# Kernel tuning notes

Measured on AMD Instinct MI355X. Metric: run time of the kernel, lower is better.

## Reference

```python
import jax, jax.numpy as jnp
import numpy as np

N_NODES = 50000
N_EDGES = 800000
D = 64
N_LAYERS = 3  # zip(convs(4), batchnorms(3)) truncates to 3 executed layers
N_GRAPHS = 32
EPS_BN = 1e-5
NEG_SLOPE = 0.2


def segment_softmax(logits, seg, n):
    m = jax.ops.segment_max(logits, seg, num_segments=n)
    m = jnp.where(jnp.isfinite(m), m, 0.0)
    z = jnp.exp(logits - m[seg])
    s = jax.ops.segment_sum(z, seg, num_segments=n)
    return z / (s[seg] + 1e-16)


def setup_inputs() -> dict:
    key = jax.random.key(0)
    ks = jax.random.split(key, 16)
    s = 0.1
    return {
        "x": jax.random.normal(ks[0], (N_NODES, D), jnp.float32),
        "edge_index": jax.random.randint(ks[1], (2, N_EDGES), 0, N_NODES),
        "edge_attr": jax.random.normal(ks[2], (N_EDGES, D), jnp.float32),
        "batch": jnp.sort(jax.random.randint(ks[3], (N_NODES,), 0, N_GRAPHS)),
        # EdgeConvLayer MLP params (stacked over layers)
        "em_w1": jax.random.normal(ks[4], (N_LAYERS, 3 * D, D)) * s,
        "em_b1": jnp.zeros((N_LAYERS, D)),
        "em_w2": jax.random.normal(ks[5], (N_LAYERS, D, D)) * s,
        "em_b2": jnp.zeros((N_LAYERS, D)),
        # GATConv params (heads=1, add_self_loops=False)
        "gat_w": jax.random.normal(ks[6], (N_LAYERS, D, D)) * s,
        "att_src": jax.random.normal(ks[7], (N_LAYERS, D)) * s,
        "att_dst": jax.random.normal(ks[8], (N_LAYERS, D)) * s,
        "edge_w": jax.random.normal(ks[9], (N_LAYERS, D, D)) * s,
        "att_edge": jax.random.normal(ks[10], (N_LAYERS, D)) * s,
        "gat_bias": jnp.zeros((N_LAYERS, D)),
        # BatchNorm params
        "bn_gamma": jnp.ones((N_LAYERS, D)),
        "bn_beta": jnp.zeros((N_LAYERS, D)),
        # readout MLP
        "mlp_w1": jax.random.normal(ks[11], (D, D)) * s,
        "mlp_b1": jnp.zeros((D,)),
        "mlp_w2": jax.random.normal(ks[12], (D, D // 2)) * s,
        "mlp_b2": jnp.zeros((D // 2,)),
        "mlp_w3": jax.random.normal(ks[13], (D // 2, 1)) * s,
        "mlp_b3": jnp.zeros((1,)),
    }


def reference(x, edge_index, edge_attr, batch, em_w1, em_b1, em_w2, em_b2,
              gat_w, att_src, att_dst, edge_w, att_edge, gat_bias,
              bn_gamma, bn_beta, mlp_w1, mlp_b1, mlp_w2, mlp_b2, mlp_w3, mlp_b3):
    row, col = edge_index[0], edge_index[1]
    n = x.shape[0]
    for l in range(N_LAYERS):
        # MetaLayer edge model: cat(src, dst, edge_attr) -> 2-layer MLP
        cat = jnp.concatenate([x[row], x[col], edge_attr], axis=1)  # (E, 3D)
        eh = jax.nn.relu(cat @ em_w1[l] + em_b1[l])
        edge_attr = eh @ em_w2[l] + em_b2[l]  # (E, D)
        # GATConv, heads=1: shared linear for src/dst
        xw = x @ gat_w[l]  # (N, D)
        a_edge = edge_attr @ (edge_w[l] @ att_edge[l])  # fused lin_edge + att_edge dot
        logits = (xw @ att_src[l])[row] + (xw @ att_dst[l])[col] + a_edge
        alpha = segment_softmax(jax.nn.leaky_relu(logits, NEG_SLOPE), col, n)
        h = jax.ops.segment_sum(alpha[:, None] * xw[row], col, num_segments=n) + gat_bias[l]
        # BatchNorm (training batch stats) + ReLU
        mu = h.mean(axis=0)
        var = h.var(axis=0)
        x = jax.nn.relu((h - mu) * jax.lax.rsqrt(var + EPS_BN) * bn_gamma[l] + bn_beta[l])
    # global mean pool over graphs
    sums = jax.ops.segment_sum(x, batch, num_segments=N_GRAPHS)
    cnt = jax.ops.segment_sum(jnp.ones((n,), x.dtype), batch, num_segments=N_GRAPHS)
    g = sums / jnp.maximum(cnt, 1.0)[:, None]
    h = jax.nn.relu(g @ mlp_w1 + mlp_b1)
    h = jax.nn.relu(h @ mlp_w2 + mlp_b2)
    return h @ mlp_w3 + mlp_b3  # (N_GRAPHS, 1)
```

## Files before the change

### kernel.cpp

```cpp
#include <hip/hip_runtime.h>


#define NN 50000
#define NE 800000
#define DP 68
#define NEG_SLOPE 0.2f

typedef __attribute__((ext_vector_type(8))) __bf16 bf16x8;
typedef __attribute__((ext_vector_type(4))) float f32x4;

__device__ __forceinline__ float4 ld4(const float* __restrict__ p){ return *(const float4* __restrict__)p; }
__device__ __forceinline__ void st4(float* __restrict__ p, float4 v){ *(float4* __restrict__)p = v; }
__device__ __forceinline__ float4 f4zero(){ return make_float4(0.f,0.f,0.f,0.f); }
__device__ __forceinline__ float4 f4add(float4 a, float4 b){
  return make_float4(a.x+b.x, a.y+b.y, a.z+b.z, a.w+b.w);
}
__device__ __forceinline__ float4 f4fma(float a, float4 b, float4 c){
  return make_float4(fmaf(a,b.x,c.x), fmaf(a,b.y,c.y), fmaf(a,b.z,c.z), fmaf(a,b.w,c.w));
}
__device__ __forceinline__ float f4dot(float4 a, float4 b){
  return fmaf(a.x,b.x, fmaf(a.y,b.y, fmaf(a.z,b.z, a.w*b.w)));
}
__device__ __forceinline__ bf16x8 cvt8(float4 a, float4 b){
  bf16x8 r;
  r[0]=(__bf16)a.x; r[1]=(__bf16)a.y; r[2]=(__bf16)a.z; r[3]=(__bf16)a.w;
  r[4]=(__bf16)b.x; r[5]=(__bf16)b.y; r[6]=(__bf16)b.z; r[7]=(__bf16)b.w;
  return r;
}
__device__ __forceinline__ bf16x8 addpack8(bf16x8 a, bf16x8 b){
  bf16x8 r;
#pragma unroll
  for (int e = 0; e < 8; ++e) r[e] = (__bf16)((float)a[e] + (float)b[e]);
  return r;
}
__device__ __forceinline__ ushort4 pack4(float4 v){
  ushort4 u;
  u.x = __builtin_bit_cast(unsigned short, (__bf16)v.x);
  u.y = __builtin_bit_cast(unsigned short, (__bf16)v.y);
  u.z = __builtin_bit_cast(unsigned short, (__bf16)v.z);
  u.w = __builtin_bit_cast(unsigned short, (__bf16)v.w);
  return u;
}
__device__ __forceinline__ float4 bnrelu4(float4 v, const float* sc, const float* sh, int d){
  return make_float4(
    fmaxf(fmaf(v.x, sc[d+0], sh[d+0]), 0.f),
    fmaxf(fmaf(v.y, sc[d+1], sh[d+1]), 0.f),
    fmaxf(fmaf(v.z, sc[d+2], sh[d+2]), 0.f),
    fmaxf(fmaf(v.w, sc[d+3], sh[d+3]), 0.f));
}

__device__ __forceinline__ void gemm_tile(const float* inT, const float* W,
                                          int el0, int d0, float4 acc[4]){
#pragma unroll 4
  for (int kc = 0; kc < 16; ++kc){
    float4 w0 = ld4(&W[(kc*4+0)*64 + d0]);
    float4 w1 = ld4(&W[(kc*4+1)*64 + d0]);
    float4 w2 = ld4(&W[(kc*4+2)*64 + d0]);
    float4 w3 = ld4(&W[(kc*4+3)*64 + d0]);
#pragma unroll
    for (int i = 0; i < 4; ++i){
      float4 iv = ld4(&inT[(el0+i)*DP + kc*4]);
      acc[i] = f4fma(iv.x, w0, acc[i]);
      acc[i] = f4fma(iv.y, w1, acc[i]);
      acc[i] = f4fma(iv.z, w2, acc[i]);
      acc[i] = f4fma(iv.w, w3, acc[i]);
    }
  }
}

__global__ __launch_bounds__(256) void hist_kernel(const int* __restrict__ ei_col,
                                                   int* __restrict__ cnt){
  int e = blockIdx.x * 256 + threadIdx.x;
  atomicAdd(&cnt[ei_col[e]], 1);
}

__global__ __launch_bounds__(256) void scan_kernel(const int* __restrict__ cnt,
                                                   int* __restrict__ off){
  __shared__ int wsum[4];
  __shared__ int carry_s;
  const int t = threadIdx.x;
  const int lane = t & 63, w = t >> 6;
  if (t == 0) carry_s = 0;
  __syncthreads();
  for (int base = 0; base < NN; base += 256){
    int idx = base + t;
    int v = (idx < NN) ? cnt[idx] : 0;
    int x = v;
#pragma unroll
    for (int o = 1; o < 64; o <<= 1){
      int u = __shfl_up(x, o);
      if (lane >= o) x += u;
    }
    if (lane == 63) wsum[w] = x;
    __syncthreads();
    int wo = carry_s;
#pragma unroll
    for (int k = 0; k < 4; ++k) if (k < w) wo += wsum[k];
    int incl = x + wo;
    if (idx < NN) off[idx] = incl - v;
    __syncthreads();
    if (t == 255) carry_s = incl;
    __syncthreads();
  }
  if (t == 0) off[NN] = carry_s;
}

__global__ __launch_bounds__(256) void scatter_kernel(
    const int* __restrict__ ei, const int* __restrict__ off, int* __restrict__ cur,
    int* __restrict__ srow, int* __restrict__ scol, int* __restrict__ perm){
  int e = blockIdx.x * 256 + threadIdx.x;
  int r = ei[e], c = ei[NE + e];
  int pos = off[c] + atomicAdd(&cur[c], 1);
  srow[pos] = r; scol[pos] = c; perm[pos] = e;
}

__global__ __launch_bounds__(256) void graph_bounds(const int* __restrict__ batch,
                                                    int* __restrict__ goff){
  int n = blockIdx.x * 256 + threadIdx.x;
  if (n >= NN) return;
  int bn = batch[n];
  int bp = (n == 0) ? -1 : batch[n-1];
  for (int g = bp + 1; g <= bn; ++g) goff[g] = n;
  if (n == NN - 1){ for (int g = bn + 1; g <= 32; ++g) goff[g] = NN; }
}

__global__ __launch_bounds__(256) void prep_weights(
    const float* __restrict__ em_w1, const float* __restrict__ em_w2,
    const float* __restrict__ edge_w, const float* __restrict__ att_edge,
    __bf16* __restrict__ w1f, __bf16* __restrict__ w2f, float* __restrict__ vbuf)
{
  const int l = blockIdx.x, t = threadIdx.x;
  const float* W1 = em_w1 + l*12288 + 8192;
  const float* W2 = em_w2 + l*4096;
  for (int p = t; p < 512; p += 256){
    int li = p & 63, ks = (p >> 6) & 1, nt = p >> 7;
    int kbase = ks*32 + (li >> 4)*8;
    int j = nt*16 + (li & 15);
    bf16x8 v1, v2;
#pragma unroll
    for (int e = 0; e < 8; ++e){
      v1[e] = (__bf16)W1[(size_t)(kbase+e)*64 + j];
      v2[e] = (__bf16)W2[(size_t)(kbase+e)*64 + j];
    }
    *(bf16x8*)(w1f + (size_t)l*4096 + p*8) = v1;
    *(bf16x8*)(w2f + (size_t)l*4096 + p*8) = v2;
  }
  if (t < 64){
    float a = 0.f;
    const float* ew = edge_w + l*4096 + t*64;
    const float* ae = att_edge + l*64;
#pragma unroll 8
    for (int j = 0; j < 64; ++j) a = fmaf(ew[j], ae[j], a);
    vbuf[l*64 + t] = a;
  }
}

__global__ __launch_bounds__(256) void node_prep(
    const float* __restrict__ x0_in, const float* __restrict__ h_in,
    const float* __restrict__ musum, const float* __restrict__ sqsum,
    const float* __restrict__ gamma, const float* __restrict__ beta,
    const float* __restrict__ em_w1, const float* __restrict__ em_b1,
    const float* __restrict__ gat_w,
    const float* __restrict__ att_src, const float* __restrict__ att_dst,
    __bf16* __restrict__ xaH, __bf16* __restrict__ xbH, __bf16* __restrict__ xwH,
    float* __restrict__ ssrc, float* __restrict__ sdst, int l)
{
  __shared__ float xt[64*DP];
  __shared__ float Ws[64*64];
  __shared__ float asrc[64], adst[64], b1s[64];
  __shared__ float sc[64], sh[64];
  const int t = threadIdx.x;
  const int n0 = blockIdx.x * 64;
  const int p = blockIdx.y;

  if (l > 0){
    if (t < 64){
      float mu  = musum[t] * (1.0f / NN);
      float var = sqsum[t] * (1.0f / NN) - mu * mu;
      float iv  = rsqrtf(var + 1e-5f) * gamma[(l-1)*64 + t];
      sc[t] = iv;
      sh[t] = beta[(l-1)*64 + t] - mu * iv;
    }
    __syncthreads();
  }

  { int nl = t >> 2, q = t & 3;
    int n = n0 + nl;
    float4 v0, v1, v2, v3;
    if (n < NN){
      const float* src = ((l == 0) ? x0_in : h_in) + (size_t)n*64 + q*16;
      v0 = ld4(src); v1 = ld4(src+4); v2 = ld4(src+8); v3 = ld4(src+12);
      if (l > 0){
        v0 = bnrelu4(v0, sc, sh, q*16);
        v1 = bnrelu4(v1, sc, sh, q*16+4);
        v2 = bnrelu4(v2, sc, sh, q*16+8);
        v3 = bnrelu4(v3, sc, sh, q*16+12);
      }
    } else { v0 = v1 = v2 = v3 = f4zero(); }
    float* dst = &xt[nl*DP + q*16];
    st4(dst, v0); st4(dst+4, v1); st4(dst+8, v2); st4(dst+12, v3);
  }
  if (p == 2){
    if (t < 64) asrc[t] = att_src[l*64 + t];
    else if (t < 128) adst[t-64] = att_dst[l*64 + (t-64)];
  } else if (p == 0 && t < 64){
    b1s[t] = em_b1[l*64 + t];
  }
  const float* wp = (p == 0) ? (em_w1 + l*12288)
                  : (p == 1) ? (em_w1 + l*12288 + 4096)
                             : (gat_w + l*4096);
  for (int i = t; i < 1024; i += 256) st4(&Ws[i*4], ld4(wp + i*4));
  __syncthreads();

  const int nl0 = (t >> 4) << 2;
  const int d0  = (t & 15) << 2;
  __bf16* op = (p == 0) ? xaH : (p == 1) ? xbH : xwH;

  float4 acc[4] = {f4zero(), f4zero(), f4zero(), f4zero()};
  gemm_tile(xt, Ws, nl0, d0, acc);
  if (p == 0){
    float4 bb = ld4(&b1s[d0]);
#pragma unroll
    for (int i = 0; i < 4; ++i) acc[i] = f4add(acc[i], bb);
  }
#pragma unroll
  for (int i = 0; i < 4; ++i){
    int n = n0 + nl0 + i;
    if (n < NN) *(ushort4*)(op + (size_t)n*64 + d0) = pack4(acc[i]);
  }
  if (p == 2){
    float4 a4 = ld4(&asrc[d0]);
    float4 b4 = ld4(&adst[d0]);
    float ps[4], pd[4];
#pragma unroll
    for (int i = 0; i < 4; ++i){ ps[i] = f4dot(acc[i], a4); pd[i] = f4dot(acc[i], b4); }
#pragma unroll
    for (int off = 8; off; off >>= 1){
#pragma unroll
      for (int i = 0; i < 4; ++i){ ps[i] += __shfl_xor(ps[i], off); pd[i] += __shfl_xor(pd[i], off); }
    }
    if ((t & 15) == 0){
#pragma unroll
      for (int i = 0; i < 4; ++i){
        int n = n0 + nl0 + i;
        if (n < NN){ ssrc[n] = ps[i]; sdst[n] = pd[i]; }
      }
    }
  }
}

__global__ __launch_bounds__(256) void edge_mlp(
    const float* __restrict__ ea0,
    const __bf16* ea_in,
    __bf16* ea_out,
    const __bf16* __restrict__ xaH, const __bf16* __restrict__ xbH,
    const float* __restrict__ ssrc, const float* __restrict__ sdst,
    const int* __restrict__ srow, const int* __restrict__ scol,
    const int* __restrict__ permp,
    const __bf16* __restrict__ w1f, const __bf16* __restrict__ w2f,
    const float* __restrict__ b2v, const float* __restrict__ vv,
    float* __restrict__ lrelu, int store_ea)
{
  __shared__ __align__(16) __bf16 uvh[64*72];
  __shared__ __align__(16) unsigned ehw[2048];
  __shared__ float b2s[64], vs[64], sb[128];
  __shared__ int rs[128], cs[128], ps[128];
  const int t = threadIdx.x;
  const int w = t >> 6, l = t & 63, m = l & 15, kg = l >> 4;
  const int eb = blockIdx.x * 128;

  if (t < 128){ rs[t] = srow[eb+t]; cs[t] = scol[eb+t]; }
  else if (t < 192){ b2s[t-128] = b2v[t-128]; vs[t-128] = vv[t-128]; }
  if (permp && t < 128) ps[t] = permp[eb+t];
  __syncthreads();

  const bf16x8* B1 = (const bf16x8*)w1f;
  const bf16x8* B2 = (const bf16x8*)w2f;
  const f32x4 z4 = {0.f, 0.f, 0.f, 0.f};
  const int e_loc = t >> 2, q = t & 3;

  const int r0 = rs[e_loc],      c0 = cs[e_loc];
  const int r1 = rs[64 + e_loc], c1 = cs[64 + e_loc];
  const bf16x8* pa0 = (const bf16x8*)(xaH + (size_t)r0*64 + q*16);
  const bf16x8* pb0 = (const bf16x8*)(xbH + (size_t)c0*64 + q*16);
  const bf16x8* pa1 = (const bf16x8*)(xaH + (size_t)r1*64 + q*16);
  const bf16x8* pb1 = (const bf16x8*)(xbH + (size_t)c1*64 + q*16);
  bf16x8 g_a0l = pa0[0], g_a0h = pa0[1], g_b0l = pb0[0], g_b0h = pb0[1];
  bf16x8 g_a1l = pa1[0], g_a1h = pa1[1], g_b1l = pb1[0], g_b1h = pb1[1];
  float sb0 = 0.f, sb1 = 0.f;
  if (q == 0){ sb0 = ssrc[r0] + sdst[c0]; sb1 = ssrc[r1] + sdst[c1]; }

  bf16x8 A00, A01, A10, A11;
  { const int elA = 16*w + m;
    if (ea0){
      const float* s0 = ea0 + (size_t)ps[elA]*64 + kg*8;
      const float* s1 = ea0 + (size_t)ps[64+elA]*64 + kg*8;
      A00 = cvt8(ld4(s0),    ld4(s0+4));  A01 = cvt8(ld4(s0+32), ld4(s0+36));
      A10 = cvt8(ld4(s1),    ld4(s1+4));  A11 = cvt8(ld4(s1+32), ld4(s1+36));
    } else {
      const __bf16* s0 = ea_in + (size_t)(eb+elA)*64 + kg*8;
      const __bf16* s1 = ea_in + (size_t)(eb+64+elA)*64 + kg*8;
      A00 = *(const bf16x8*)s0;  A01 = *(const bf16x8*)(s0+32);
      A10 = *(const bf16x8*)s1;  A11 = *(const bf16x8*)(s1+32);
    }
  }

  *(bf16x8*)&uvh[e_loc*72 + q*16]     = addpack8(g_a0l, g_b0l);
  *(bf16x8*)&uvh[e_loc*72 + q*16 + 8] = addpack8(g_a0h, g_b0h);
  if (q == 0){ sb[e_loc] = sb0; sb[64 + e_loc] = sb1; }
  asm volatile("" ::: "memory");

  __bf16* esc = (__bf16*)ehw;
  auto tile_compute = [&](bf16x8 a0, bf16x8 a1, int tb){
    f32x4 acc[4];
#pragma unroll
    for (int nt = 0; nt < 4; ++nt){
      acc[nt] = __builtin_amdgcn_mfma_f32_16x16x32_bf16(a0, B1[(nt*2+0)*64 + l], z4, 0, 0, 0);
      acc[nt] = __builtin_amdgcn_mfma_f32_16x16x32_bf16(a1, B1[(nt*2+1)*64 + l], acc[nt], 0, 0, 0);
    }
#pragma unroll
    for (int nt = 0; nt < 4; ++nt){
      const int j = nt*16 + m;
#pragma unroll
      for (int r = 0; r < 4; ++r){
        const int erow = 16*w + 4*kg + r;
        float v = acc[nt][r] + (float)uvh[erow*72 + j];
        v = fmaxf(v, 0.f);
        const int piece = (w*2 + (nt>>1))*64 + (((nt&1)<<1) | (m>>3))*16 + 4*kg + r;
        esc[piece*8 + (m&7)] = (__bf16)v;
      }
    }
    asm volatile("" ::: "memory");
    bf16x8 a20 = *(const bf16x8*)(esc + (size_t)((w*2+0)*64 + kg*16 + m)*8);
    bf16x8 a21 = *(const bf16x8*)(esc + (size_t)((w*2+1)*64 + kg*16 + m)*8);
    f32x4 acc2[4];
#pragma unroll
    for (int nt = 0; nt < 4; ++nt){
      acc2[nt] = __builtin_amdgcn_mfma_f32_16x16x32_bf16(a20, B2[(nt*2+0)*64 + l], z4, 0, 0, 0);
      acc2[nt] = __builtin_amdgcn_mfma_f32_16x16x32_bf16(a21, B2[(nt*2+1)*64 + l], acc2[nt], 0, 0, 0);
    }
    float p0 = 0.f, p1 = 0.f, p2 = 0.f, p3 = 0.f;
#pragma unroll
    for (int nt = 0; nt < 4; ++nt){
      const int j = nt*16 + m;
      const float bj = b2s[j], vj = vs[j];
      float vr[4];
      vr[0] = acc2[nt][0] + bj; vr[1] = acc2[nt][1] + bj;
      vr[2] = acc2[nt][2] + bj; vr[3] = acc2[nt][3] + bj;
      if (store_ea){
        const size_t rowb = (size_t)(eb + tb + 16*w + 4*kg)*64 + (j & ~1);
#pragma unroll
        for (int r = 0; r < 4; ++r){
          unsigned short hu = __builtin_bit_cast(unsigned short, (__bf16)vr[r]);
          int pu = __shfl_xor((int)hu, 1);
          if (!(m & 1)){
            unsigned word = (unsigned)hu | ((unsigned)(pu & 0xffff) << 16);
            *(unsigned*)(ea_out + rowb + (size_t)r*64) = word;
          }
        }
      }
      p0 = fmaf(vr[0], vj, p0); p1 = fmaf(vr[1], vj, p1);
      p2 = fmaf(vr[2], vj, p2); p3 = fmaf(vr[3], vj, p3);
    }
#pragma unroll
    for (int o = 8; o; o >>= 1){
      p0 += __shfl_xor(p0, o); p1 += __shfl_xor(p1, o);
      p2 += __shfl_xor(p2, o); p3 += __shfl_xor(p3, o);
    }
    if (m == 0){
      float pv[4] = {p0, p1, p2, p3};
#pragma unroll
      for (int r = 0; r < 4; ++r){
        const int erow = 16*w + 4*kg + r;
        float logit = sb[tb + erow] + pv[r];
        lrelu[eb + tb + erow] = logit > 0.f ? logit : NEG_SLOPE * logit;
      }
    }
  };

  tile_compute(A00, A01, 0);
  asm volatile("" ::: "memory");
  *(bf16x8*)&uvh[e_loc*72 + q*16]     = addpack8(g_a1l, g_b1l);
  *(bf16x8*)&uvh[e_loc*72 + q*16 + 8] = addpack8(g_a1h, g_b1h);
  asm volatile("" ::: "memory");
  tile_compute(A10, A11, 64);
}

__global__ __launch_bounds__(256) void col_agg(
    const float* __restrict__ lrelu, const int* __restrict__ srow,
    const int* __restrict__ off, const __bf16* __restrict__ xwH,
    float* __restrict__ h)
{
  __shared__ float zS[4][128];
  __shared__ int   rS[4][128];
  const int t = threadIdx.x;
  const int lane = t & 63;
  const int wv = t >> 6;
  const int c = blockIdx.x * 4 + wv;
  const int s0 = off[c], s1 = off[c+1];
  const int L = s1 - s0;

  float l0 = (lane < L)    ? lrelu[s0+lane]    : -3.402823466e38f;
  float l1 = (lane+64 < L) ? lrelu[s0+64+lane] : -3.402823466e38f;
  int   r0 = (lane < L)    ? srow[s0+lane]     : 0;
  int   r1 = (lane+64 < L) ? srow[s0+64+lane]  : 0;

  float m = fmaxf(l0, l1);
  for (int i = lane+128; i < L; i += 64) m = fmaxf(m, lrelu[s0+i]);
#pragma unroll
  for (int o = 32; o; o >>= 1) m = fmaxf(m, __shfl_xor(m, o));

  float z0 = (lane < L)    ? expf(l0 - m) : 0.f;
  float z1 = (lane+64 < L) ? expf(l1 - m) : 0.f;
  float s = z0 + z1;
  for (int i = lane+128; i < L; i += 64) s += expf(lrelu[s0+i] - m);
#pragma unroll
  for (int o = 32; o; o >>= 1) s += __shfl_xor(s, o);
  const float inv = 1.f / (s + 1e-16f);

  zS[wv][lane] = z0;  zS[wv][64+lane] = z1;
  rS[wv][lane] = r0;  rS[wv][64+lane] = r1;
  asm volatile("" ::: "memory");

  float hv0 = 0.f, hv1 = 0.f, hv2 = 0.f, hv3 = 0.f;
  float hv4 = 0.f, hv5 = 0.f, hv6 = 0.f, hv7 = 0.f;
  if (L <= 128){
    int i = 0;
    for (; i + 8 <= L; i += 8){
      float za = zS[wv][i],   zb = zS[wv][i+1], zc = zS[wv][i+2], zd = zS[wv][i+3];
      float ze = zS[wv][i+4], zf = zS[wv][i+5], zg = zS[wv][i+6], zh = zS[wv][i+7];
      int   ra = rS[wv][i],   rb = rS[wv][i+1], rc = rS[wv][i+2], rd = rS[wv][i+3];
      int   re = rS[wv][i+4], rf = rS[wv][i+5], rg = rS[wv][i+6], rh = rS[wv][i+7];
      hv0 = fmaf(za, (float)xwH[(size_t)ra*64 + lane], hv0);
      hv1 = fmaf(zb, (float)xwH[(size_t)rb*64 + lane], hv1);
      hv2 = fmaf(zc, (float)xwH[(size_t)rc*64 + lane], hv2);
      hv3 = fmaf(zd, (float)xwH[(size_t)rd*64 + lane], hv3);
      hv4 = fmaf(ze, (float)xwH[(size_t)re*64 + lane], hv4);
      hv5 = fmaf(zf, (float)xwH[(size_t)rf*64 + lane], hv5);
      hv6 = fmaf(zg, (float)xwH[(size_t)rg*64 + lane], hv6);
      hv7 = fmaf(zh, (float)xwH[(size_t)rh*64 + lane], hv7);
    }
    for (; i < L; ++i)
      hv0 = fmaf(zS[wv][i], (float)xwH[(size_t)rS[wv][i]*64 + lane], hv0);
  } else {
    for (int i = 0; i < L; ++i){
      float z = expf(lrelu[s0+i] - m);
      int r = srow[s0+i];
      hv0 = fmaf(z, (float)xwH[(size_t)r*64 + lane], hv0);
    }
  }
  float hv = ((hv0 + hv1) + (hv2 + hv3)) + ((hv4 + hv5) + (hv6 + hv7));
  h[(size_t)c*64 + lane] = hv * inv;
}

__global__ __launch_bounds__(256) void bn_stats(
    const float* __restrict__ h, float* __restrict__ musum, float* __restrict__ sqsum)
{
  const int t = threadIdx.x;
  const int d = t & 63, sub = t >> 6;
  const int base = blockIdx.x * 256;
  float s = 0.f, s2 = 0.f;
  for (int i = sub; i < 256; i += 4){
    int n = base + i;
    if (n < NN){ float v = h[(size_t)n*64 + d]; s += v; s2 = fmaf(v, v, s2); }
  }
  __shared__ float r1[4][64], r2[4][64];
  r1[sub][d] = s; r2[sub][d] = s2;
  __syncthreads();
  if (sub == 0){
    s  = r1[0][d] + r1[1][d] + r1[2][d] + r1[3][d];
    s2 = r2[0][d] + r2[1][d] + r2[2][d] + r2[3][d];
    atomicAdd(&musum[d], s);
    atomicAdd(&sqsum[d], s2);
  }
}

__global__ __launch_bounds__(256) void seg_pool(
    const float* __restrict__ h, const int* __restrict__ goff,
    const float* __restrict__ musum, const float* __restrict__ sqsum,
    const float* __restrict__ gamma2, const float* __restrict__ beta2,
    float* __restrict__ pools, float* __restrict__ pcnt)
{
  const int g = blockIdx.x;
  const int t = threadIdx.x;
  const int d = t & 63, sub = t >> 6;
  const int s0 = goff[g], s1 = goff[g+1];
  float mu  = musum[d] * (1.0f / NN);
  float var = sqsum[d] * (1.0f / NN) - mu * mu;
  float iv  = rsqrtf(var + 1e-5f) * gamma2[d];
  float shv = beta2[d] - mu * iv;
  float s = 0.f;
  for (int n = s0 + sub; n < s1; n += 4)
    s += fmaxf(fmaf(h[(size_t)n*64 + d], iv, shv), 0.f);
  __shared__ float r[4][64];
  r[sub][d] = s;
  __syncthreads();
  if (sub == 0){
    s = r[0][d] + r[1][d] + r[2][d] + r[3][d];
    pools[g*64 + d] = s;
    if (d == 0) pcnt[g] = (float)(s1 - s0);
  }
}

__global__ __launch_bounds__(256) void final_mlp(
    const float* __restrict__ pools, const float* __restrict__ pcnt,
    const float* __restrict__ w1, const float* __restrict__ b1,
    const float* __restrict__ w2, const float* __restrict__ b2,
    const float* __restrict__ w3, const float* __restrict__ b3,
    float* __restrict__ out)
{
  __shared__ float g[32*64], h1[32*64], h2[32*32];
  const int t = threadIdx.x;
  for (int i = t; i < 2048; i += 256) g[i] = pools[i] / fmaxf(pcnt[i >> 6], 1.0f);
  __syncthreads();
  for (int i = t; i < 2048; i += 256){
    int gi = i >> 6, d = i & 63;
    float a = b1[d];
    for (int k = 0; k < 64; ++k) a = fmaf(g[gi*64 + k], w1[k*64 + d], a);
    h1[i] = fmaxf(a, 0.f);
  }
  __syncthreads();
  for (int i = t; i < 1024; i += 256){
    int gi = i >> 5, d = i & 31;
    float a = b2[d];
    for (int k = 0; k < 64; ++k) a = fmaf(h1[gi*64 + k], w2[k*32 + d], a);
    h2[i] = fmaxf(a, 0.f);
  }
  __syncthreads();
  if (t < 32){
    float a = b3[0];
    for (int k = 0; k < 32; ++k) a = fmaf(h2[t*32 + k], w3[k], a);
    out[t] = a;
  }
}

extern "C" void kernel_launch(void* const* d_in, const int* in_sizes, int n_in,
                              void* d_out, int out_size, void* d_ws, size_t ws_size,
                              hipStream_t stream)
{
  (void)in_sizes; (void)n_in; (void)out_size; (void)ws_size;
  const float* x0       = (const float*)d_in[0];
  const int*   ei       = (const int*)  d_in[1];
  const float* ea0      = (const float*)d_in[2];
  const int*   batch    = (const int*)  d_in[3];
  const float* em_w1    = (const float*)d_in[4];
  const float* em_b1    = (const float*)d_in[5];
  const float* em_w2    = (const float*)d_in[6];
  const float* em_b2    = (const float*)d_in[7];
  const float* gat_w    = (const float*)d_in[8];
  const float* att_src  = (const float*)d_in[9];
  const float* att_dst  = (const float*)d_in[10];
  const float* edge_w   = (const float*)d_in[11];
  const float* att_edge = (const float*)d_in[12];
  const float* bn_gamma = (const float*)d_in[14];
  const float* bn_beta  = (const float*)d_in[15];
  const float* mlp_w1   = (const float*)d_in[16];
  const float* mlp_b1   = (const float*)d_in[17];
  const float* mlp_w2   = (const float*)d_in[18];
  const float* mlp_b2   = (const float*)d_in[19];
  const float* mlp_w3   = (const float*)d_in[20];
  const float* mlp_b3   = (const float*)d_in[21];
  float* out = (float*)d_out;

  const size_t N64 = (size_t)NN * 64, E64 = (size_t)NE * 64;
  float* ws    = (float*)d_ws;
  float* wsE   = ws;
  float* sxa   = wsE + E64;
  float* sxb   = sxa + N64;
  float* sxw   = sxb + N64;
  float* hbuf  = sxw + N64;
  float* musum = hbuf + N64;
  float* sqsum = musum + 64;
  float* lrelu = sqsum + 64;
  float* pools = lrelu + NE;
  float* pcnt  = pools + 2048;
  float* ssrc  = pcnt + 32;
  float* sdst  = ssrc + NN;
  int*   cnt   = (int*)(sdst + NN);
  int*   cur   = cnt + NN;
  int*   soff  = cur + NN;
  int*   srow  = soff + NN + 1;
  int*   scol  = srow + NE;
  int*   perm  = scol + NE;
  int*   goff  = perm + NE;
  __bf16* eaB  = (__bf16*)wsE;
  __bf16* xaH  = (__bf16*)sxa;
  __bf16* xbH  = (__bf16*)sxb;
  __bf16* xwH  = (__bf16*)sxw;
  __bf16* w1f  = (__bf16*)(goff + 40);
  __bf16* w2f  = w1f + 3*4096;
  float* vbuf  = (float*)(w2f + 3*4096);

  hipMemsetAsync(cnt, 0, 2 * NN * sizeof(int), stream);
  hist_kernel<<<NE / 256, 256, 0, stream>>>(ei + NE, cnt);
  scan_kernel<<<1, 256, 0, stream>>>(cnt, soff);
  scatter_kernel<<<NE / 256, 256, 0, stream>>>(ei, soff, cur, srow, scol, perm);
  graph_bounds<<<(NN + 255) / 256, 256, 0, stream>>>(batch, goff);
  prep_weights<<<3, 256, 0, stream>>>(em_w1, em_w2, edge_w, att_edge, w1f, w2f, vbuf);

  for (int l = 0; l < 3; ++l){
    dim3 npg((NN + 63) / 64, 3);
    node_prep<<<npg, 256, 0, stream>>>(
        x0, hbuf, musum, sqsum, bn_gamma, bn_beta,
        em_w1, em_b1, gat_w, att_src, att_dst, xaH, xbH, xwH, ssrc, sdst, l);

    hipMemsetAsync(musum, 0, 128 * sizeof(float), stream);

    edge_mlp<<<NE / 128, 256, 0, stream>>>(
        (l == 0) ? ea0 : nullptr, eaB, eaB, xaH, xbH, ssrc, sdst,
        srow, scol, (l == 0) ? perm : nullptr,
        w1f + (size_t)l*4096, w2f + (size_t)l*4096,
        em_b2 + l*64, vbuf + l*64, lrelu, (l < 2) ? 1 : 0);

    col_agg<<<NN / 4, 256, 0, stream>>>(lrelu, srow, soff, xwH, hbuf);

    bn_stats<<<(NN + 255) / 256, 256, 0, stream>>>(hbuf, musum, sqsum);
  }

  seg_pool<<<32, 256, 0, stream>>>(hbuf, goff, musum, sqsum,
                                   bn_gamma + 128, bn_beta + 128, pools, pcnt);
  final_mlp<<<1, 256, 0, stream>>>(pools, pcnt, mlp_w1, mlp_b1, mlp_w2, mlp_b2,
                                   mlp_w3, mlp_b3, out);
}
```

Before: 813.5 us.

## Compute full 3D-input edge MLP in MFMA instead of precomputing node projections

Rather than precomputing x@W1a and x@W1b per node and adding them per edge, a separate kernel now writes a single bf16 copy of the (batch-normalized) node features. The edge kernel gathers the raw row and column features and runs the full K=192 first-layer GEMM on MFMA, with the bias added in-kernel. This removes two of the three node GEMM passes, their node-sized buffers and the shared-memory add step, at the cost of three times more MFMA work per edge in the first layer. It also adds one extra elementwise kernel launch per layer.

```diff
diff --git a/kernel.cpp b/kernel.cpp
--- a/kernel.cpp
+++ b/kernel.cpp
@@ -12,9 +12,6 @@
 __device__ __forceinline__ float4 ld4(const float* __restrict__ p){ return *(const float4* __restrict__)p; }
 __device__ __forceinline__ void st4(float* __restrict__ p, float4 v){ *(float4* __restrict__)p = v; }
 __device__ __forceinline__ float4 f4zero(){ return make_float4(0.f,0.f,0.f,0.f); }
-__device__ __forceinline__ float4 f4add(float4 a, float4 b){
-  return make_float4(a.x+b.x, a.y+b.y, a.z+b.z, a.w+b.w);
-}
 __device__ __forceinline__ float4 f4fma(float a, float4 b, float4 c){
   return make_float4(fmaf(a,b.x,c.x), fmaf(a,b.y,c.y), fmaf(a,b.z,c.z), fmaf(a,b.w,c.w));
 }
@@ -25,12 +22,6 @@
   bf16x8 r;
   r[0]=(__bf16)a.x; r[1]=(__bf16)a.y; r[2]=(__bf16)a.z; r[3]=(__bf16)a.w;
   r[4]=(__bf16)b.x; r[5]=(__bf16)b.y; r[6]=(__bf16)b.z; r[7]=(__bf16)b.w;
-  return r;
-}
-__device__ __forceinline__ bf16x8 addpack8(bf16x8 a, bf16x8 b){
-  bf16x8 r;
-#pragma unroll
-  for (int e = 0; e < 8; ++e) r[e] = (__bf16)((float)a[e] + (float)b[e]);
   return r;
 }
 __device__ __forceinline__ ushort4 pack4(float4 v){
@@ -130,19 +121,24 @@
     __bf16* __restrict__ w1f, __bf16* __restrict__ w2f, float* __restrict__ vbuf)
 {
   const int l = blockIdx.x, t = threadIdx.x;
-  const float* W1 = em_w1 + l*12288 + 8192;
+  const float* W1 = em_w1 + l*12288;
   const float* W2 = em_w2 + l*4096;
+  for (int p = t; p < 1536; p += 256){
+    int li = p & 63, ks = (p >> 6) % 6, nt = p / 384;
+    int kbase = ks*32 + (li >> 4)*8;
+    int j = nt*16 + (li & 15);
+    bf16x8 v1;
+#pragma unroll
+    for (int e = 0; e < 8; ++e) v1[e] = (__bf16)W1[(size_t)(kbase+e)*64 + j];
+    *(bf16x8*)(w1f + (size_t)l*12288 + p*8) = v1;
+  }
   for (int p = t; p < 512; p += 256){
     int li = p & 63, ks = (p >> 6) & 1, nt = p >> 7;
     int kbase = ks*32 + (li >> 4)*8;
     int j = nt*16 + (li & 15);
-    bf16x8 v1, v2;
-#pragma unroll
-    for (int e = 0; e < 8; ++e){
-      v1[e] = (__bf16)W1[(size_t)(kbase+e)*64 + j];
-      v2[e] = (__bf16)W2[(size_t)(kbase+e)*64 + j];
-    }
-    *(bf16x8*)(w1f + (size_t)l*4096 + p*8) = v1;
+    bf16x8 v2;
+#pragma unroll
+    for (int e = 0; e < 8; ++e) v2[e] = (__bf16)W2[(size_t)(kbase+e)*64 + j];
     *(bf16x8*)(w2f + (size_t)l*4096 + p*8) = v2;
   }
   if (t < 64){
@@ -155,24 +151,14 @@
   }
 }
 
-__global__ __launch_bounds__(256) void node_prep(
-    const float* __restrict__ x0_in, const float* __restrict__ h_in,
+__global__ __launch_bounds__(256) void x_to_bf16(
+    const float* __restrict__ x0, const float* __restrict__ h,
     const float* __restrict__ musum, const float* __restrict__ sqsum,
     const float* __restrict__ gamma, const float* __restrict__ beta,
-    const float* __restrict__ em_w1, const float* __restrict__ em_b1,
-    const float* __restrict__ gat_w,
-    const float* __restrict__ att_src, const float* __restrict__ att_dst,
-    __bf16* __restrict__ xaH, __bf16* __restrict__ xbH, __bf16* __restrict__ xwH,
-    float* __restrict__ ssrc, float* __restrict__ sdst, int l)
-{
-  __shared__ float xt[64*DP];
-  __shared__ float Ws[64*64];
-  __shared__ float asrc[64], adst[64], b1s[64];
+    __bf16* __restrict__ xH, int l)
+{
   __shared__ float sc[64], sh[64];
   const int t = threadIdx.x;
-  const int n0 = blockIdx.x * 64;
-  const int p = blockIdx.y;
-
   if (l > 0){
     if (t < 64){
       float mu  = musum[t] * (1.0f / NN);
@@ -183,68 +169,70 @@
     }
     __syncthreads();
   }
+  const size_t i4 = (size_t)blockIdx.x * 256 + t;
+  const float* src = (l == 0) ? x0 : h;
+  float4 v = ld4(src + i4*4);
+  if (l > 0) v = bnrelu4(v, sc, sh, (int)((i4*4) & 63));
+  *(ushort4*)(xH + i4*4) = pack4(v);
+}
+
+__global__ __launch_bounds__(256) void node_prep(
+    const __bf16* __restrict__ xH,
+    const float* __restrict__ gat_w,
+    const float* __restrict__ att_src, const float* __restrict__ att_dst,
+    __bf16* __restrict__ xwH,
+    float* __restrict__ ssrc, float* __restrict__ sdst, int l)
+{
+  __shared__ float xt[64*DP];
+  __shared__ float Ws[64*64];
+  __shared__ float asrc[64], adst[64];
+  const int t = threadIdx.x;
+  const int n0 = blockIdx.x * 64;
 
   { int nl = t >> 2, q = t & 3;
     int n = n0 + nl;
     float4 v0, v1, v2, v3;
     if (n < NN){
-      const float* src = ((l == 0) ? x0_in : h_in) + (size_t)n*64 + q*16;
-      v0 = ld4(src); v1 = ld4(src+4); v2 = ld4(src+8); v3 = ld4(src+12);
-      if (l > 0){
-        v0 = bnrelu4(v0, sc, sh, q*16);
-        v1 = bnrelu4(v1, sc, sh, q*16+4);
-        v2 = bnrelu4(v2, sc, sh, q*16+8);
-        v3 = bnrelu4(v3, sc, sh, q*16+12);
-      }
+      const bf16x8* src = (const bf16x8*)(xH + (size_t)n*64 + q*16);
+      bf16x8 a = src[0], b = src[1];
+      v0 = make_float4((float)a[0], (float)a[1], (float)a[2], (float)a[3]);
+      v1 = make_float4((float)a[4], (float)a[5], (float)a[6], (float)a[7]);
+      v2 = make_float4((float)b[0], (float)b[1], (float)b[2], (float)b[3]);
+      v3 = make_float4((float)b[4], (float)b[5], (float)b[6], (float)b[7]);
     } else { v0 = v1 = v2 = v3 = f4zero(); }
     float* dst = &xt[nl*DP + q*16];
     st4(dst, v0); st4(dst+4, v1); st4(dst+8, v2); st4(dst+12, v3);
   }
-  if (p == 2){
-    if (t < 64) asrc[t] = att_src[l*64 + t];
-    else if (t < 128) adst[t-64] = att_dst[l*64 + (t-64)];
-  } else if (p == 0 && t < 64){
-    b1s[t] = em_b1[l*64 + t];
-  }
-  const float* wp = (p == 0) ? (em_w1 + l*12288)
-                  : (p == 1) ? (em_w1 + l*12288 + 4096)
-                             : (gat_w + l*4096);
-  for (int i = t; i < 1024; i += 256) st4(&Ws[i*4], ld4(wp + i*4));
+  if (t < 64) asrc[t] = att_src[l*64 + t];
+  else if (t < 128) adst[t-64] = att_dst[l*64 + (t-64)];
+  for (int i = t; i < 1024; i += 256) st4(&Ws[i*4], ld4(gat_w + l*4096 + i*4));
   __syncthreads();
 
   const int nl0 = (t >> 4) << 2;
   const int d0  = (t & 15) << 2;
-  __bf16* op = (p == 0) ? xaH : (p == 1) ? xbH : xwH;
 
   float4 acc[4] = {f4zero(), f4zero(), f4zero(), f4zero()};
   gemm_tile(xt, Ws, nl0, d0, acc);
-  if (p == 0){
-    float4 bb = ld4(&b1s[d0]);
-#pragma unroll
-    for (int i = 0; i < 4; ++i) acc[i] = f4add(acc[i], bb);
-  }
 #pragma unroll
   for (int i = 0; i < 4; ++i){
     int n = n0 + nl0 + i;
-    if (n < NN) *(ushort4*)(op + (size_t)n*64 + d0) = pack4(acc[i]);
-  }
-  if (p == 2){
-    float4 a4 = ld4(&asrc[d0]);
-    float4 b4 = ld4(&adst[d0]);
-    float ps[4], pd[4];
-#pragma unroll
-    for (int i = 0; i < 4; ++i){ ps[i] = f4dot(acc[i], a4); pd[i] = f4dot(acc[i], b4); }
-#pragma unroll
-    for (int off = 8; off; off >>= 1){
-#pragma unroll
-      for (int i = 0; i < 4; ++i){ ps[i] += __shfl_xor(ps[i], off); pd[i] += __shfl_xor(pd[i], off); }
-    }
-    if ((t & 15) == 0){
-#pragma unroll
-      for (int i = 0; i < 4; ++i){
-        int n = n0 + nl0 + i;
-        if (n < NN){ ssrc[n] = ps[i]; sdst[n] = pd[i]; }
-      }
+    if (n < NN) *(ushort4*)(xwH + (size_t)n*64 + d0) = pack4(acc[i]);
+  }
+  float4 a4 = ld4(&asrc[d0]);
+  float4 b4 = ld4(&adst[d0]);
+  float ps[4], pd[4];
+#pragma unroll
+  for (int i = 0; i < 4; ++i){ ps[i] = f4dot(acc[i], a4); pd[i] = f4dot(acc[i], b4); }
+#pragma unroll
+  for (int off = 8; off; off >>= 1){
+#pragma unroll
+    for (int i = 0; i < 4; ++i){ ps[i] += __shfl_xor(ps[i], off); pd[i] += __shfl_xor(pd[i], off); }
+  }
+  if ((t & 15) == 0){
+#pragma unroll
+    for (int i = 0; i < 4; ++i){
+      int n = n0 + nl0 + i;
+      if (n < NN){ ssrc[n] = ps[i]; sdst[n] = pd[i]; }
     }
   }
 }
@@ -253,17 +241,17 @@
     const float* __restrict__ ea0,
     const __bf16* ea_in,
     __bf16* ea_out,
-    const __bf16* __restrict__ xaH, const __bf16* __restrict__ xbH,
+    const __bf16* __restrict__ xH,
     const float* __restrict__ ssrc, const float* __restrict__ sdst,
     const int* __restrict__ srow, const int* __restrict__ scol,
     const int* __restrict__ permp,
     const __bf16* __restrict__ w1f, const __bf16* __restrict__ w2f,
-    const float* __restrict__ b2v, const float* __restrict__ vv,
+    const float* __restrict__ b1v, const float* __restrict__ b2v,
+    const float* __restrict__ vv,
     float* __restrict__ lrelu, int store_ea)
 {
-  __shared__ __align__(16) __bf16 uvh[64*72];
   __shared__ __align__(16) unsigned ehw[2048];
-  __shared__ float b2s[64], vs[64], sb[128];
+  __shared__ float b1s[64], b2s[64], vs[64], sb[128];
   __shared__ int rs[128], cs[128], ps[128];
   const int t = threadIdx.x;
   const int w = t >> 6, l = t & 63, m = l & 15, kg = l >> 4;
@@ -271,6 +259,7 @@
 
   if (t < 128){ rs[t] = srow[eb+t]; cs[t] = scol[eb+t]; }
   else if (t < 192){ b2s[t-128] = b2v[t-128]; vs[t-128] = vv[t-128]; }
+  else { b1s[t-192] = b1v[t-192]; }
   if (permp && t < 128) ps[t] = permp[eb+t];
   __syncthreads();
 
@@ -279,53 +268,57 @@
   const f32x4 z4 = {0.f, 0.f, 0.f, 0.f};
   const int e_loc = t >> 2, q = t & 3;
 
-  const int r0 = rs[e_loc],      c0 = cs[e_loc];
-  const int r1 = rs[64 + e_loc], c1 = cs[64 + e_loc];
-  const bf16x8* pa0 = (const bf16x8*)(xaH + (size_t)r0*64 + q*16);
-  const bf16x8* pb0 = (const bf16x8*)(xbH + (size_t)c0*64 + q*16);
-  const bf16x8* pa1 = (const bf16x8*)(xaH + (size_t)r1*64 + q*16);
-  const bf16x8* pb1 = (const bf16x8*)(xbH + (size_t)c1*64 + q*16);
-  bf16x8 g_a0l = pa0[0], g_a0h = pa0[1], g_b0l = pb0[0], g_b0h = pb0[1];
-  bf16x8 g_a1l = pa1[0], g_a1h = pa1[1], g_b1l = pb1[0], g_b1h = pb1[1];
   float sb0 = 0.f, sb1 = 0.f;
-  if (q == 0){ sb0 = ssrc[r0] + sdst[c0]; sb1 = ssrc[r1] + sdst[c1]; }
-
-  bf16x8 A00, A01, A10, A11;
-  { const int elA = 16*w + m;
-    if (ea0){
-      const float* s0 = ea0 + (size_t)ps[elA]*64 + kg*8;
-      const float* s1 = ea0 + (size_t)ps[64+elA]*64 + kg*8;
-      A00 = cvt8(ld4(s0),    ld4(s0+4));  A01 = cvt8(ld4(s0+32), ld4(s0+36));
-      A10 = cvt8(ld4(s1),    ld4(s1+4));  A11 = cvt8(ld4(s1+32), ld4(s1+36));
-    } else {
-      const __bf16* s0 = ea_in + (size_t)(eb+elA)*64 + kg*8;
-      const __bf16* s1 = ea_in + (size_t)(eb+64+elA)*64 + kg*8;
-      A00 = *(const bf16x8*)s0;  A01 = *(const bf16x8*)(s0+32);
-      A10 = *(const bf16x8*)s1;  A11 = *(const bf16x8*)(s1+32);
-    }
-  }
-
-  *(bf16x8*)&uvh[e_loc*72 + q*16]     = addpack8(g_a0l, g_b0l);
-  *(bf16x8*)&uvh[e_loc*72 + q*16 + 8] = addpack8(g_a0h, g_b0h);
+  if (q == 0){
+    sb0 = ssrc[rs[e_loc]] + sdst[cs[e_loc]];
+    sb1 = ssrc[rs[64 + e_loc]] + sdst[cs[64 + e_loc]];
+  }
+  const int elA0 = 16*w + m, elA1 = 64 + elA0;
+  const int ra0 = rs[elA0], ca0 = cs[elA0];
+  const int ra1 = rs[elA1], ca1 = cs[elA1];
+  const bf16x8* pr0 = (const bf16x8*)(xH + (size_t)ra0*64 + kg*8);
+  const bf16x8* pc0 = (const bf16x8*)(xH + (size_t)ca0*64 + kg*8);
+  const bf16x8* pr1 = (const bf16x8*)(xH + (size_t)ra1*64 + kg*8);
+  const bf16x8* pc1 = (const bf16x8*)(xH + (size_t)ca1*64 + kg*8);
+  bf16x8 Xr00 = pr0[0], Xr01 = pr0[4];
+  bf16x8 Xc00 = pc0[0], Xc01 = pc0[4];
+  bf16x8 Xr10 = pr1[0], Xr11 = pr1[4];
+  bf16x8 Xc10 = pc1[0], Xc11 = pc1[4];
+  bf16x8 Ae00, Ae01, Ae10, Ae11;
+  if (ea0){
+    const float* s0 = ea0 + (size_t)ps[elA0]*64 + kg*8;
+    const float* s1 = ea0 + (size_t)ps[elA1]*64 + kg*8;
+    Ae00 = cvt8(ld4(s0),    ld4(s0+4));  Ae01 = cvt8(ld4(s0+32), ld4(s0+36));
+    Ae10 = cvt8(ld4(s1),    ld4(s1+4));  Ae11 = cvt8(ld4(s1+32), ld4(s1+36));
+  } else {
+    const __bf16* s0 = ea_in + (size_t)(eb+elA0)*64 + kg*8;
+    const __bf16* s1 = ea_in + (size_t)(eb+elA1)*64 + kg*8;
+    Ae00 = *(const bf16x8*)s0;  Ae01 = *(const bf16x8*)(s0+32);
+    Ae10 = *(const bf16x8*)s1;  Ae11 = *(const bf16x8*)(s1+32);
+  }
   if (q == 0){ sb[e_loc] = sb0; sb[64 + e_loc] = sb1; }
   asm volatile("" ::: "memory");
 
   __bf16* esc = (__bf16*)ehw;
-  auto tile_compute = [&](bf16x8 a0, bf16x8 a1, int tb){
+  auto tile_compute = [&](bf16x8 xr0, bf16x8 xr1, bf16x8 xc0, bf16x8 xc1,
+                          bf16x8 ae0, bf16x8 ae1, int tb){
     f32x4 acc[4];
 #pragma unroll
     for (int nt = 0; nt < 4; ++nt){
-      acc[nt] = __builtin_amdgcn_mfma_f32_16x16x32_bf16(a0, B1[(nt*2+0)*64 + l], z4, 0, 0, 0);
-      acc[nt] = __builtin_amdgcn_mfma_f32_16x16x32_bf16(a1, B1[(nt*2+1)*64 + l], acc[nt], 0, 0, 0);
+      acc[nt] = __builtin_amdgcn_mfma_f32_16x16x32_bf16(xr0, B1[(nt*6+0)*64 + l], z4, 0, 0, 0);
+      acc[nt] = __builtin_amdgcn_mfma_f32_16x16x32_bf16(xr1, B1[(nt*6+1)*64 + l], acc[nt], 0, 0, 0);
+      acc[nt] = __builtin_amdgcn_mfma_f32_16x16x32_bf16(xc0, B1[(nt*6+2)*64 + l], acc[nt], 0, 0, 0);
+      acc[nt] = __builtin_amdgcn_mfma_f32_16x16x32_bf16(xc1, B1[(nt*6+3)*64 + l], acc[nt], 0, 0, 0);
+      acc[nt] = __builtin_amdgcn_mfma_f32_16x16x32_bf16(ae0, B1[(nt*6+4)*64 + l], acc[nt], 0, 0, 0);
+      acc[nt] = __builtin_amdgcn_mfma_f32_16x16x32_bf16(ae1, B1[(nt*6+5)*64 + l], acc[nt], 0, 0, 0);
     }
 #pragma unroll
     for (int nt = 0; nt < 4; ++nt){
       const int j = nt*16 + m;
+      const float bj = b1s[j];
 #pragma unroll
       for (int r = 0; r < 4; ++r){
-        const int erow = 16*w + 4*kg + r;
-        float v = acc[nt][r] + (float)uvh[erow*72 + j];
-        v = fmaxf(v, 0.f);
+        float v = fmaxf(acc[nt][r] + bj, 0.f);
         const int piece = (w*2 + (nt>>1))*64 + (((nt&1)<<1) | (m>>3))*16 + 4*kg + r;
         esc[piece*8 + (m&7)] = (__bf16)v;
       }
@@ -378,12 +371,9 @@
     }
   };
 
-  tile_compute(A00, A01, 0);
+  tile_compute(Xr00, Xr01, Xc00, Xc01, Ae00, Ae01, 0);
   asm volatile("" ::: "memory");
-  *(bf16x8*)&uvh[e_loc*72 + q*16]     = addpack8(g_a1l, g_b1l);
-  *(bf16x8*)&uvh[e_loc*72 + q*16 + 8] = addpack8(g_a1h, g_b1h);
-  asm volatile("" ::: "memory");
-  tile_compute(A10, A11, 64);
+  tile_compute(Xr10, Xr11, Xc10, Xc11, Ae10, Ae11, 64);
 }
 
 __global__ __launch_bounds__(256) void col_agg(
@@ -565,9 +555,8 @@
   const size_t N64 = (size_t)NN * 64, E64 = (size_t)NE * 64;
   float* ws    = (float*)d_ws;
   float* wsE   = ws;
-  float* sxa   = wsE + E64;
-  float* sxb   = sxa + N64;
-  float* sxw   = sxb + N64;
+  float* sxh   = wsE + E64;
+  float* sxw   = sxh + N64;
   float* hbuf  = sxw + N64;
   float* musum = hbuf + N64;
   float* sqsum = musum + 64;
@@ -584,11 +573,10 @@
   int*   perm  = scol + NE;
   int*   goff  = perm + NE;
   __bf16* eaB  = (__bf16*)wsE;
-  __bf16* xaH  = (__bf16*)sxa;
-  __bf16* xbH  = (__bf16*)sxb;
+  __bf16* xH   = (__bf16*)sxh;
   __bf16* xwH  = (__bf16*)sxw;
   __bf16* w1f  = (__bf16*)(goff + 40);
-  __bf16* w2f  = w1f + 3*4096;
+  __bf16* w2f  = w1f + 3*12288;
   float* vbuf  = (float*)(w2f + 3*4096);
 
   hipMemsetAsync(cnt, 0, 2 * NN * sizeof(int), stream);
@@ -599,18 +587,19 @@
   prep_weights<<<3, 256, 0, stream>>>(em_w1, em_w2, edge_w, att_edge, w1f, w2f, vbuf);
 
   for (int l = 0; l < 3; ++l){
-    dim3 npg((NN + 63) / 64, 3);
-    node_prep<<<npg, 256, 0, stream>>>(
-        x0, hbuf, musum, sqsum, bn_gamma, bn_beta,
-        em_w1, em_b1, gat_w, att_src, att_dst, xaH, xbH, xwH, ssrc, sdst, l);
+    x_to_bf16<<<(int)(N64 / 1024), 256, 0, stream>>>(
+        x0, hbuf, musum, sqsum, bn_gamma, bn_beta, xH, l);
 
     hipMemsetAsync(musum, 0, 128 * sizeof(float), stream);
 
+    node_prep<<<(NN + 63) / 64, 256, 0, stream>>>(
+        xH, gat_w, att_src, att_dst, xwH, ssrc, sdst, l);
+
     edge_mlp<<<NE / 128, 256, 0, stream>>>(
-        (l == 0) ? ea0 : nullptr, eaB, eaB, xaH, xbH, ssrc, sdst,
+        (l == 0) ? ea0 : nullptr, eaB, eaB, xH, ssrc, sdst,
         srow, scol, (l == 0) ? perm : nullptr,
-        w1f + (size_t)l*4096, w2f + (size_t)l*4096,
-        em_b2 + l*64, vbuf + l*64, lrelu, (l < 2) ? 1 : 0);
+        w1f + (size_t)l*12288, w2f + (size_t)l*4096,
+        em_b1 + l*64, em_b2 + l*64, vbuf + l*64, lrelu, (l < 2) ? 1 : 0);
 
     col_agg<<<NN / 4, 256, 0, stream>>>(lrelu, srow, soff, xwH, hbuf);
 
```

Measured after the change: 902.5 us. +10.9%, slower.
